# Kernel tuning notes

Measured on AMD Instinct MI355X. Metric: run time of the kernel, lower is better.

Reference implementation:

```python
import jax, jax.numpy as jnp
import numpy as np


def _local2d(x, weight, stride, padding):
    """Locally-connected 2D conv: per-output-location filters.
    x: [N, C, H, W], weight: [h_out, w_out, O, C, k, k].
    Returns [N, O, h_out, w_out].
    """
    h_out, w_out, O, C, k, _ = weight.shape
    if padding > 0:
        x = jnp.pad(x, ((0, 0), (0, 0), (padding, padding), (padding, padding)))
    # Gather all k x k windows at once (no python loop over locations).
    ih = (jnp.arange(h_out) * stride)[:, None] + jnp.arange(k)[None, :]  # [h_out, k]
    iw = (jnp.arange(w_out) * stride)[:, None] + jnp.arange(k)[None, :]  # [w_out, k]
    # patches: [N, C, h_out, w_out, k, k]
    patches = x[:, :, ih[:, None, :, None], iw[None, :, None, :]]
    # out[n,o,h,w] = sum_{c,p,q} weight[h,w,o,c,p,q] * patches[n,c,h,w,p,q]
    return jnp.einsum('hwocpq,nchwpq->nohw', weight, patches)


def setup_inputs() -> dict:
    key = jax.random.key(0)
    k1, k2 = jax.random.split(key)
    B, CAT, C, H, W = 32, 10, 32, 32, 32
    O, K, STRIDE, PAD = 64, 3, 1, 1
    h_out = (H + 2 * PAD - K) // STRIDE + 1
    w_out = (W + 2 * PAD - K) // STRIDE + 1
    x = jax.random.normal(k1, (B, CAT, C, H, W), dtype=jnp.float32)
    # init_local with first_layer=False, mono=False: std = 1/sqrt(0.5*C*K^2)
    std = 1.0 / np.sqrt(0.5 * C * K ** 2)
    weight = jax.random.normal(k2, (h_out, w_out, O, C, K, K), dtype=jnp.float32) * std
    bias = jnp.zeros((CAT, O, h_out, w_out), dtype=jnp.float32)
    return {"x": x, "weight": weight, "bias": bias}


def reference(x, weight, bias):
    STRIDE, PAD = 1, 1
    B, CAT = x.shape[:2]
    x_flat = x.reshape((B * CAT,) + x.shape[2:])            # [B*CAT, C, H, W]
    out_flat = _local2d(x_flat, weight, STRIDE, PAD)        # [B*CAT, O, h_out, w_out]
    out = out_flat.reshape((B, CAT) + out_flat.shape[1:])   # [B, CAT, O, h_out, w_out]
    return out + bias[None]
```

## Files before the change

kernel.cpp:

```cpp
#include <hip/hip_runtime.h>
#include <hip/hip_bf16.h>


typedef __attribute__((ext_vector_type(8))) short short8;
typedef __attribute__((ext_vector_type(4))) float f32x4;
typedef __attribute__((ext_vector_type(4))) unsigned short ushort4b;

#define XT2_ELEMS 10485760
#define ZSLAB_ELEMS 10240
#define OUTS_OFF_BYTES 20992000

__device__ __forceinline__ unsigned short f2bf(float f) {
    __hip_bfloat16 b = __float2bfloat16(f);
    return __builtin_bit_cast(unsigned short, b);
}

__global__ __launch_bounds__(256) void VecLocal2d_xpose(const float* __restrict__ x,
                                                        unsigned short* __restrict__ xT2) {
    __shared__ unsigned short tile[64][68];
    if (blockIdx.x == 0) {
#pragma unroll
        for (int j = 0; j < 20; ++j)
            reinterpret_cast<unsigned int*>(xT2 + XT2_ELEMS)[threadIdx.x + j * 256] = 0u;
    }
    const int mcb = blockIdx.x >> 4;
    const int yxb = blockIdx.x & 15;
    const int t = threadIdx.x;
    const int g = t >> 4;
    const int l4 = (t & 15) * 4;
#pragma unroll
    for (int p = 0; p < 4; ++p) {
        const int ml = g + p * 16;
        const float4 v = *reinterpret_cast<const float4*>(
            x + (size_t)(mcb * 64 + ml) * 1024 + yxb * 64 + l4);
        ushort4b u;
        u.x = f2bf(v.x); u.y = f2bf(v.y); u.z = f2bf(v.z); u.w = f2bf(v.w);
        *reinterpret_cast<ushort4b*>(&tile[ml][l4]) = u;
    }
    __syncthreads();
#pragma unroll
    for (int p = 0; p < 4; ++p) {
        const int yl = g + p * 16;
        ushort4b u;
        u.x = tile[l4 + 0][yl];
        u.y = tile[l4 + 1][yl];
        u.z = tile[l4 + 2][yl];
        u.w = tile[l4 + 3][yl];
        *reinterpret_cast<ushort4b*>(xT2 + (size_t)(yxb * 64 + yl) * 10240 + mcb * 64 + l4) = u;
    }
}

__global__ __launch_bounds__(256, 4) void VecLocal2d_main(const unsigned short* __restrict__ xT2,
                                                          const float* __restrict__ weight,
                                                          float* __restrict__ out_s) {
    __shared__ unsigned short wLDS[64 * 296];

    const int bid = blockIdx.x;
    const int s = bid >> 7;
    const int hg = bid & 127;
    const int h = hg >> 2;
    const int w = ((hg & 3) << 3) | s;
    const int loc = h * 32 + w;

    const int tid = threadIdx.x;
    const int lane = tid & 63;
    const int wave = tid >> 6;
    const int quad = lane >> 4;
    const int l16 = lane & 15;
    const int wm = wave >> 1, wn = wave & 1;

    const float* wg = weight + (size_t)loc * 18432;
#pragma unroll
    for (int i = 0; i < 18; ++i) {
        const int f4i = tid + i * 256;
        const float4 v = reinterpret_cast<const float4*>(wg)[f4i];
        const int o = f4i / 72;
        const int kbase = (f4i - o * 72) * 4;
        const float vv[4] = {v.x, v.y, v.z, v.w};
#pragma unroll
        for (int e = 0; e < 4; ++e) {
            const int k = kbase + e;
            const int c = k / 9;
            const int r = k - c * 9;
            wLDS[o * 296 + r * 32 + c] = f2bf(vv[e]);
        }
    }

    int base[9];
#pragma unroll
    for (int dy = 0; dy < 3; ++dy)
#pragma unroll
        for (int dx = 0; dx < 3; ++dx) {
            const int y = h - 1 + dy;
            const int xc = w - 1 + dx;
            const bool valid = ((unsigned)y < 32u) && ((unsigned)xc < 32u);
            base[dy * 3 + dx] = valid ? (y * 32 + xc) * 10240 : XT2_ELEMS;
        }

    __syncthreads();

    short8 bfr[2][9];
#pragma unroll
    for (int tni = 0; tni < 2; ++tni) {
        const int o = (wn * 2 + tni) * 16 + l16;
#pragma unroll
        for (int kt = 0; kt < 9; ++kt)
            bfr[tni][kt] = *reinterpret_cast<const short8*>(&wLDS[o * 296 + kt * 32 + quad * 8]);
    }

    const int laneA = (wm * 32 + l16) * 32 + quad * 8;
    float* os = out_s + (size_t)loc * 20480;

    for (int mt = 0; mt < 5; ++mt) {
        const int moff = laneA + mt * 2048;
        f32x4 acc[2][2] = {};
#pragma unroll
        for (int kt = 0; kt < 9; ++kt) {
            const short8 a0 = *reinterpret_cast<const short8*>(xT2 + base[kt] + moff);
            const short8 a1 = *reinterpret_cast<const short8*>(xT2 + base[kt] + moff + 512);
            acc[0][0] = __builtin_amdgcn_mfma_f32_16x16x32_bf16(a0, bfr[0][kt], acc[0][0], 0, 0, 0);
            acc[0][1] = __builtin_amdgcn_mfma_f32_16x16x32_bf16(a0, bfr[1][kt], acc[0][1], 0, 0, 0);
            acc[1][0] = __builtin_amdgcn_mfma_f32_16x16x32_bf16(a1, bfr[0][kt], acc[1][0], 0, 0, 0);
            acc[1][1] = __builtin_amdgcn_mfma_f32_16x16x32_bf16(a1, bfr[1][kt], acc[1][1], 0, 0, 0);
        }

#pragma unroll
        for (int tmi = 0; tmi < 2; ++tmi)
#pragma unroll
            for (int tni = 0; tni < 2; ++tni) {
                const int o = (wn * 2 + tni) * 16 + l16;
#pragma unroll
                for (int r = 0; r < 4; ++r) {
                    const int m = mt * 64 + (wm * 2 + tmi) * 16 + quad * 4 + r;
                    os[m * 64 + o] = acc[tmi][tni][r];
                }
            }
    }
}

__global__ __launch_bounds__(256) void VecLocal2d_outT(const float* __restrict__ out_s,
                                                       const float* __restrict__ bias,
                                                       float* __restrict__ out) {
    __shared__ float tile[64][65];
    const int m = blockIdx.x >> 4;
    const int loc0 = (blockIdx.x & 15) * 64;
    const int t = threadIdx.x;
    const float* src = out_s + (size_t)loc0 * 20480 + m * 64;
#pragma unroll
    for (int p = 0; p < 4; ++p) {
        const int idx = p * 256 + t;
        const int lr = idx >> 4;
        const int c4 = (idx & 15) * 4;
        const float4 v = *reinterpret_cast<const float4*>(src + (size_t)lr * 20480 + c4);
        tile[lr][c4 + 0] = v.x; tile[lr][c4 + 1] = v.y;
        tile[lr][c4 + 2] = v.z; tile[lr][c4 + 3] = v.w;
    }
    __syncthreads();
    const int cat = m % 10;
#pragma unroll
    for (int p = 0; p < 4; ++p) {
        const int idx = p * 256 + t;
        const int o = idx >> 4;
        const int l4 = (idx & 15) * 4;
        const float4 bv = *reinterpret_cast<const float4*>(
            bias + ((size_t)(cat * 64 + o)) * 1024 + loc0 + l4);
        float4 v;
        v.x = tile[l4 + 0][o] + bv.x;
        v.y = tile[l4 + 1][o] + bv.y;
        v.z = tile[l4 + 2][o] + bv.z;
        v.w = tile[l4 + 3][o] + bv.w;
        *reinterpret_cast<float4*>(out + ((size_t)(m * 64 + o)) * 1024 + loc0 + l4) = v;
    }
}

extern "C" void kernel_launch(void* const* d_in, const int* in_sizes, int n_in,
                              void* d_out, int out_size, void* d_ws, size_t ws_size,
                              hipStream_t stream) {
    const float* x = (const float*)d_in[0];
    const float* wgt = (const float*)d_in[1];
    const float* bias = (const float*)d_in[2];
    float* out = (float*)d_out;
    unsigned short* xT2 = (unsigned short*)d_ws;
    float* out_s = (float*)((char*)d_ws + OUTS_OFF_BYTES);

    VecLocal2d_xpose<<<2560, 256, 0, stream>>>(x, xT2);
    VecLocal2d_main<<<1024, 256, 0, stream>>>(xT2, wgt, out_s);
    VecLocal2d_outT<<<5120, 256, 0, stream>>>(out_s, bias, out);
}
```

Baseline: 224.4 us.

## Fuse output transpose and bias add into main MFMA kernel with XCD-aware block mapping

Removes the intermediate out_s buffer and the separate transpose/bias kernel. The main kernel now adds bias staged in LDS and writes straight to the final [B,CAT,O,H,W] layout. Block IDs are remapped so that 16 consecutive spatial locations run on the same XCD, so the scattered per-location stores can merge in L2. This saves a full write plus read of the intermediate tensor and one launch, at the cost of uncoalesced 4-byte stores with a 4KB stride. Launch bounds are also lowered to 3 blocks/SM.

```diff
diff --git a/kernel.cpp b/kernel.cpp
--- a/kernel.cpp
+++ b/kernel.cpp
@@ -8,7 +8,6 @@
 
 #define XT2_ELEMS 10485760
 #define ZSLAB_ELEMS 10240
-#define OUTS_OFF_BYTES 20992000
 
 __device__ __forceinline__ unsigned short f2bf(float f) {
     __hip_bfloat16 b = __float2bfloat16(f);
@@ -50,17 +49,22 @@
     }
 }
 
-__global__ __launch_bounds__(256, 4) void VecLocal2d_main(const unsigned short* __restrict__ xT2,
+__global__ __launch_bounds__(256, 3) void VecLocal2d_main(const unsigned short* __restrict__ xT2,
                                                           const float* __restrict__ weight,
-                                                          float* __restrict__ out_s) {
+                                                          const float* __restrict__ bias,
+                                                          float* __restrict__ out) {
     __shared__ unsigned short wLDS[64 * 296];
+    __shared__ float biasLDS[10 * 65];
 
     const int bid = blockIdx.x;
-    const int s = bid >> 7;
-    const int hg = bid & 127;
-    const int h = hg >> 2;
-    const int w = ((hg & 3) << 3) | s;
-    const int loc = h * 32 + w;
+    const int xcd = bid & 7;
+    const int i = bid >> 3;
+    const int slot = i >> 4;
+    const int k16 = i & 15;
+    const int grp = slot * 8 + xcd;
+    const int loc = grp * 16 + k16;
+    const int h = loc >> 5;
+    const int w = loc & 31;
 
     const int tid = threadIdx.x;
     const int lane = tid & 63;
@@ -71,8 +75,8 @@
 
     const float* wg = weight + (size_t)loc * 18432;
 #pragma unroll
-    for (int i = 0; i < 18; ++i) {
-        const int f4i = tid + i * 256;
+    for (int i2 = 0; i2 < 18; ++i2) {
+        const int f4i = tid + i2 * 256;
         const float4 v = reinterpret_cast<const float4*>(wg)[f4i];
         const int o = f4i / 72;
         const int kbase = (f4i - o * 72) * 4;
@@ -84,6 +88,12 @@
             const int r = k - c * 9;
             wLDS[o * 296 + r * 32 + c] = f2bf(vv[e]);
         }
+    }
+
+    for (int i2 = tid; i2 < 640; i2 += 256) {
+        const int cat = i2 >> 6;
+        const int o = i2 & 63;
+        biasLDS[cat * 65 + o] = bias[((size_t)(cat * 64 + o)) * 1024 + loc];
     }
 
     int base[9];
@@ -109,7 +119,9 @@
     }
 
     const int laneA = (wm * 32 + l16) * 32 + quad * 8;
-    float* os = out_s + (size_t)loc * 20480;
+    const int mb0 = wm * 32 + quad * 4;
+    const int cat0_0 = mb0 % 10;
+    const int cat0_1 = (mb0 + 16) % 10;
 
     for (int mt = 0; mt < 5; ++mt) {
         const int moff = laneA + mt * 2048;
@@ -124,52 +136,23 @@
             acc[1][1] = __builtin_amdgcn_mfma_f32_16x16x32_bf16(a1, bfr[1][kt], acc[1][1], 0, 0, 0);
         }
 
+        const int mt4 = mt * 4;
 #pragma unroll
-        for (int tmi = 0; tmi < 2; ++tmi)
+        for (int tmi = 0; tmi < 2; ++tmi) {
+            const int mbase = mt * 64 + (wm * 2 + tmi) * 16 + quad * 4;
+            const int cbase = (tmi ? cat0_1 : cat0_0) + mt4;
 #pragma unroll
             for (int tni = 0; tni < 2; ++tni) {
                 const int o = (wn * 2 + tni) * 16 + l16;
 #pragma unroll
                 for (int r = 0; r < 4; ++r) {
-                    const int m = mt * 64 + (wm * 2 + tmi) * 16 + quad * 4 + r;
-                    os[m * 64 + o] = acc[tmi][tni][r];
+                    int cat = cbase + r;
+                    cat -= (cat >= 20) ? 20 : ((cat >= 10) ? 10 : 0);
+                    const float v = acc[tmi][tni][r] + biasLDS[cat * 65 + o];
+                    out[((size_t)((mbase + r) * 64 + o)) * 1024 + loc] = v;
                 }
             }
-    }
-}
-
-__global__ __launch_bounds__(256) void VecLocal2d_outT(const float* __restrict__ out_s,
-                                                       const float* __restrict__ bias,
-                                                       float* __restrict__ out) {
-    __shared__ float tile[64][65];
-    const int m = blockIdx.x >> 4;
-    const int loc0 = (blockIdx.x & 15) * 64;
-    const int t = threadIdx.x;
-    const float* src = out_s + (size_t)loc0 * 20480 + m * 64;
-#pragma unroll
-    for (int p = 0; p < 4; ++p) {
-        const int idx = p * 256 + t;
-        const int lr = idx >> 4;
-        const int c4 = (idx & 15) * 4;
-        const float4 v = *reinterpret_cast<const float4*>(src + (size_t)lr * 20480 + c4);
-        tile[lr][c4 + 0] = v.x; tile[lr][c4 + 1] = v.y;
-        tile[lr][c4 + 2] = v.z; tile[lr][c4 + 3] = v.w;
-    }
-    __syncthreads();
-    const int cat = m % 10;
-#pragma unroll
-    for (int p = 0; p < 4; ++p) {
-        const int idx = p * 256 + t;
-        const int o = idx >> 4;
-        const int l4 = (idx & 15) * 4;
-        const float4 bv = *reinterpret_cast<const float4*>(
-            bias + ((size_t)(cat * 64 + o)) * 1024 + loc0 + l4);
-        float4 v;
-        v.x = tile[l4 + 0][o] + bv.x;
-        v.y = tile[l4 + 1][o] + bv.y;
-        v.z = tile[l4 + 2][o] + bv.z;
-        v.w = tile[l4 + 3][o] + bv.w;
-        *reinterpret_cast<float4*>(out + ((size_t)(m * 64 + o)) * 1024 + loc0 + l4) = v;
+        }
     }
 }
 
@@ -181,9 +164,7 @@
     const float* bias = (const float*)d_in[2];
     float* out = (float*)d_out;
     unsigned short* xT2 = (unsigned short*)d_ws;
-    float* out_s = (float*)((char*)d_ws + OUTS_OFF_BYTES);
 
     VecLocal2d_xpose<<<2560, 256, 0, stream>>>(x, xT2);
-    VecLocal2d_main<<<1024, 256, 0, stream>>>(xT2, wgt, out_s);
-    VecLocal2d_outT<<<5120, 256, 0, stream>>>(out_s, bias, out);
+    VecLocal2d_main<<<1024, 256, 0, stream>>>(xT2, wgt, bias, out);
 }
```

Measured after the change: 311.1 us. 1.39x slower.
